# Performance work log

Hardware: AMD Instinct MI355X
Metric: run time of the kernel (lower is better)

## Reference

```python
import jax, jax.numpy as jnp
import numpy as np

N = 200000      # total nodes
E = 3200000     # total edges (avg degree 16)
B = 2000        # graphs
NPG = 100       # nodes per graph (N = B*NPG)
H = 32          # hidden_channels
MAXZ = 1000     # max_z
K = 60          # sort-pool k
D = H * 3 + 1   # total_latent_dim = 97
DENSE = ((K - 2) // 2 + 1 - 5 + 1) * 32  # 832


def setup_inputs() -> dict:
    key = jax.random.key(0)
    ks = jax.random.split(key, 24)
    inp = {}
    inp['z1'] = jax.random.randint(ks[0], (N,), 0, MAXZ)
    inp['z2'] = jax.random.randint(ks[1], (N,), 0, MAXZ)
    inp['w'] = jax.random.randint(ks[2], (N,), 0, MAXZ)
    inp['edge_index'] = jax.random.randint(ks[3], (2, E), 0, N)
    inp['batch'] = jnp.arange(N) // NPG  # contiguous graph ids
    inp['edge_weight'] = jax.random.uniform(ks[4], (E,), dtype=jnp.float32)
    s = 0.1
    inp['emb_w'] = jax.random.normal(ks[5], (MAXZ, H), jnp.float32) * s
    inp['emb_z1'] = jax.random.normal(ks[6], (MAXZ, H), jnp.float32) * s
    inp['emb_z2'] = jax.random.normal(ks[7], (MAXZ, H), jnp.float32) * s
    inp['W0'] = jax.random.normal(ks[8], (3 * H, H), jnp.float32) * s
    inp['b0'] = jnp.zeros((H,), jnp.float32)
    inp['W1'] = jax.random.normal(ks[9], (H, H), jnp.float32) * s
    inp['b1'] = jnp.zeros((H,), jnp.float32)
    inp['W2'] = jax.random.normal(ks[10], (H, H), jnp.float32) * s
    inp['b2'] = jnp.zeros((H,), jnp.float32)
    inp['W3'] = jax.random.normal(ks[11], (H, 1), jnp.float32) * s
    inp['b3'] = jnp.zeros((1,), jnp.float32)
    inp['c1_W'] = jax.random.normal(ks[12], (16, 1, D), jnp.float32) * s
    inp['c1_b'] = jnp.zeros((16,), jnp.float32)
    inp['c2_W'] = jax.random.normal(ks[13], (32, 16, 5), jnp.float32) * s
    inp['c2_b'] = jnp.zeros((32,), jnp.float32)
    inp['l1_W'] = jax.random.normal(ks[14], (DENSE, 128), jnp.float32) * s
    inp['l1_b'] = jnp.zeros((128,), jnp.float32)
    inp['l2_W'] = jax.random.normal(ks[15], (128, 1), jnp.float32) * s
    inp['l2_b'] = jnp.zeros((1,), jnp.float32)
    return inp


def _gcn(x, W, b, src, dst, ew):
    # GCNConv: add self loops (weight 1), symmetric normalization, aggregate src->dst
    loop = jnp.arange(N)
    s = jnp.concatenate([src, loop])
    d = jnp.concatenate([dst, loop])
    wgt = jnp.concatenate([ew, jnp.ones((N,), ew.dtype)])
    deg = jax.ops.segment_sum(wgt, d, num_segments=N)
    dis = jnp.where(deg > 0, jax.lax.rsqrt(deg), 0.0)
    norm = dis[s] * wgt * dis[d]
    h = x @ W                                  # [N, out]
    out = jax.ops.segment_sum(norm[:, None] * h[s], d, num_segments=N)
    return out + b


def reference(z1, z2, w, edge_index, batch, edge_weight,
              emb_w, emb_z1, emb_z2,
              W0, b0, W1, b1, W2, b2, W3, b3,
              c1_W, c1_b, c2_W, c2_b, l1_W, l1_b, l2_W, l2_b):
    src, dst = edge_index[0], edge_index[1]
    x0 = jnp.concatenate([emb_w[w], emb_z1[z1], emb_z2[z2]], axis=1)  # [N, 3H]
    h1 = jnp.tanh(_gcn(x0, W0, b0, src, dst, edge_weight))
    h2 = jnp.tanh(_gcn(h1, W1, b1, src, dst, edge_weight))
    h3 = jnp.tanh(_gcn(h2, W2, b2, src, dst, edge_weight))
    h4 = jnp.tanh(_gcn(h3, W3, b3, src, dst, edge_weight))
    x = jnp.concatenate([h1, h2, h3, h4], axis=-1)  # [N, D]

    # global_sort_pool: contiguous equal-size graphs -> reshape, sort desc by last channel, top-k
    xg = x.reshape(B, NPG, D)
    order = jnp.argsort(-xg[..., -1], axis=1)[:, :K]          # [B, K]
    xk = jnp.take_along_axis(xg, order[..., None], axis=1)    # [B, K, D]

    # conv1: kernel=stride=D on flattened [B,1,K*D] == per-slot projection
    t = jax.nn.relu(jnp.einsum('bkd,od->bok', xk, c1_W[:, 0, :]) + c1_b[None, :, None])  # [B,16,K]
    t = t.reshape(B, 16, K // 2, 2).max(axis=-1)              # maxpool 2,2 -> [B,16,30]
    t = jax.lax.conv_general_dilated(t, c2_W, (1,), 'VALID',
                                     dimension_numbers=('NCH', 'OIH', 'NCH'))
    t = jax.nn.relu(t + c2_b[None, :, None])                  # [B,32,26]
    t = t.reshape(B, -1)                                      # [B, DENSE]
    t = jax.nn.relu(t @ l1_W + l1_b)
    # dropout p=0.5 skipped (eval mode)
    return t @ l2_W + l2_b                                    # [B,1]
```

## Files before the change

kernel.cpp:

```cpp
#include <hip/hip_runtime.h>
#include <math.h>

#define NPG 100
#define KTOP 60
#define DLAT 97
#define NB 2000
#define NBLK 128
#define CPB 25000

static __device__ __forceinline__ float dot4(float4 a, float4 b){
  return a.x*b.x + a.y*b.y + a.z*b.z + a.w*b.w;
}

__global__ __launch_bounds__(256) void k_hist(const int* __restrict__ dst, int* __restrict__ histG, int E){
  __shared__ int h[NB];
  int blk = blockIdx.x, tid = threadIdx.x;
  for(int i=tid;i<NB;i+=256) h[i]=0;
  __syncthreads();
  int e0 = blk*CPB, e1 = min(e0+CPB, E);
  for(int e=e0+tid; e<e1; e+=256) atomicAdd(&h[dst[e]/NPG], 1);
  __syncthreads();
  for(int i=tid;i<NB;i+=256) histG[blk*NB+i] = h[i];
}

__global__ __launch_bounds__(NBLK) void k_colscan(const int* __restrict__ histG,
    int* __restrict__ prefT, int* __restrict__ total){
  __shared__ int s[NBLK];
  int b = blockIdx.x, t = threadIdx.x;
  int v = histG[t*NB + b];
  s[t] = v;
  __syncthreads();
  for(int off=1; off<NBLK; off<<=1){
    int u = (t >= off) ? s[t-off] : 0;
    __syncthreads();
    s[t] += u;
    __syncthreads();
  }
  prefT[b*NBLK + t] = s[t] - v;
  if(t == NBLK-1) total[b] = s[t];
}

__global__ __launch_bounds__(1024) void k_bscan(const int* __restrict__ total, int* __restrict__ bbase){
  __shared__ int s[1024];
  int t = threadIdx.x;
  int i0 = 2*t, i1 = 2*t+1;
  int x0 = (i0 < NB) ? total[i0] : 0;
  int x1 = (i1 < NB) ? total[i1] : 0;
  int ps = x0 + x1;
  s[t] = ps;
  __syncthreads();
  for(int off=1; off<1024; off<<=1){
    int u = (t >= off) ? s[t-off] : 0;
    __syncthreads();
    s[t] += u;
    __syncthreads();
  }
  int excl = s[t] - ps;
  if(i0 < NB) bbase[i0] = excl;
  if(i1 < NB) bbase[i1] = excl + x0;
  if(t == 1023) bbase[NB] = s[1023];
}

__global__ __launch_bounds__(256) void k_scatter(const int* __restrict__ src, const int* __restrict__ dst,
    const float* __restrict__ ew, const int* __restrict__ prefT, const int* __restrict__ bbase,
    int2* __restrict__ ebuf, int E){
  __shared__ int cur[NB];
  int blk = blockIdx.x, tid = threadIdx.x;
  for(int i=tid;i<NB;i+=256) cur[i] = prefT[i*NBLK + blk] + bbase[i];
  __syncthreads();
  int e0 = blk*CPB, e1 = min(e0+CPB, E);
  for(int e=e0+tid; e<e1; e+=256){
    int d = dst[e];
    int b = d/NPG;
    int dmod = d - b*NPG;
    int pos = atomicAdd(&cur[b], 1);
    ebuf[pos] = make_int2(src[e] | (dmod<<18), __float_as_int(ew[e]));
  }
}

__global__ __launch_bounds__(256) void k_bucket(const int2* __restrict__ ebuf, const int* __restrict__ bbase,
    float* __restrict__ dis, int* __restrict__ rs, int2* __restrict__ csr, int N){
  __shared__ float degw[NPG];
  __shared__ int cnt[NPG];
  __shared__ int cur[NPG];
  __shared__ int sc[128];
  int g = blockIdx.x, tid = threadIdx.x;
  int g0 = g*NPG;
  if(tid < NPG){ degw[tid] = 0.f; cnt[tid] = 0; }
  __syncthreads();
  int e0 = bbase[g], e1 = bbase[g+1];
  for(int e=e0+tid; e<e1; e+=256){
    int2 t = ebuf[e];
    int ld = ((unsigned)t.x)>>18;
    atomicAdd(&cnt[ld], 1);
    atomicAdd(&degw[ld], __int_as_float(t.y));
  }
  __syncthreads();
  if(tid < NPG) dis[g0+tid] = rsqrtf(degw[tid] + 1.0f);
  if(tid < 128) sc[tid] = (tid < NPG) ? cnt[tid] : 0;
  __syncthreads();
  for(int off=1; off<128; off<<=1){
    int u = 0;
    if(tid < 128 && tid >= off) u = sc[tid-off];
    __syncthreads();
    if(tid < 128) sc[tid] += u;
    __syncthreads();
  }
  if(tid < NPG){
    int st = e0 + sc[tid] - cnt[tid];
    cur[tid] = st;
    rs[g0+tid] = st;
  }
  if(g == NB-1 && tid == 0) rs[N] = e1;
  __syncthreads();
  for(int e=e0+tid; e<e1; e+=256){
    int2 t = ebuf[e];
    int ld = ((unsigned)t.x)>>18;
    int pos = atomicAdd(&cur[ld], 1);
    csr[pos] = make_int2(t.x & 0x3FFFF, t.y);
  }
}

__global__ __launch_bounds__(256) void k_gemm1(const int* __restrict__ wI, const int* __restrict__ z1I,
   const int* __restrict__ z2I,
   const float* __restrict__ embw, const float* __restrict__ embz1, const float* __restrict__ embz2,
   const float* __restrict__ W0, const float* __restrict__ dis, float* __restrict__ gx, int N){
  __shared__ __align__(16) float X[128][97];
  __shared__ __align__(16) float Ws[96*32];
  __shared__ int iw[128], i1[128], i2[128];
  int tid = threadIdx.x;
  int g0 = blockIdx.x*128;
  for(int i=tid;i<768;i+=256) ((float4*)Ws)[i] = ((const float4*)W0)[i];
  if(tid < 128){
    int gn = g0 + tid;
    bool ok = gn < N;
    iw[tid] = ok ? wI[gn]  : 0;
    i1[tid] = ok ? z1I[gn] : 0;
    i2[tid] = ok ? z2I[gn] : 0;
  }
  __syncthreads();
  for(int r=0;r<48;r++){
    int flat = r*256 + tid;
    int n = flat/96, c = flat - n*96;
    int gn = g0 + n;
    float val = 0.f;
    if(gn < N){
      if(c < 32)      val = embw [iw[n]*32 + c];
      else if(c < 64) val = embz1[i1[n]*32 + (c-32)];
      else            val = embz2[i2[n]*32 + (c-64)];
    }
    X[n][c] = val;
  }
  __syncthreads();
  int ng = tid>>3, chg = tid&7;
  float4 acc[4];
  #pragma unroll
  for(int j=0;j<4;j++) acc[j] = make_float4(0.f,0.f,0.f,0.f);
  #pragma unroll 4
  for(int i=0;i<96;i++){
    float4 wv = *(const float4*)&Ws[i*32 + chg*4];
    #pragma unroll
    for(int j=0;j<4;j++){
      float xv = X[ng*4+j][i];
      acc[j].x += xv*wv.x; acc[j].y += xv*wv.y; acc[j].z += xv*wv.z; acc[j].w += xv*wv.w;
    }
  }
  #pragma unroll
  for(int j=0;j<4;j++){
    int gn = g0 + ng*4 + j;
    if(gn < N){
      float dv = dis[gn];
      acc[j].x *= dv; acc[j].y *= dv; acc[j].z *= dv; acc[j].w *= dv;
      *(float4*)&gx[(size_t)gn*32 + chg*4] = acc[j];
    }
  }
}

__global__ __launch_bounds__(256) void k_gemm32(const float* __restrict__ xin, const float* __restrict__ W,
    const float* __restrict__ dis, float* __restrict__ gx, int N){
  __shared__ __align__(16) float X[128][33];
  __shared__ __align__(16) float Ws[32*32];
  int tid = threadIdx.x;
  int g0 = blockIdx.x*128;
  ((float4*)Ws)[tid] = ((const float4*)W)[tid];
  for(int r=0;r<4;r++){
    int f = r*256 + tid;
    int n = f>>3, c4 = f&7;
    int gn = g0 + n;
    float4 v = (gn < N) ? ((const float4*)(xin + (size_t)gn*32))[c4] : make_float4(0,0,0,0);
    float* xr = &X[n][c4*4];
    xr[0]=v.x; xr[1]=v.y; xr[2]=v.z; xr[3]=v.w;
  }
  __syncthreads();
  int ng = tid>>3, chg = tid&7;
  float4 acc[4];
  #pragma unroll
  for(int j=0;j<4;j++) acc[j] = make_float4(0.f,0.f,0.f,0.f);
  #pragma unroll 4
  for(int i=0;i<32;i++){
    float4 wv = *(const float4*)&Ws[i*32 + chg*4];
    #pragma unroll
    for(int j=0;j<4;j++){
      float xv = X[ng*4+j][i];
      acc[j].x += xv*wv.x; acc[j].y += xv*wv.y; acc[j].z += xv*wv.z; acc[j].w += xv*wv.w;
    }
  }
  #pragma unroll
  for(int j=0;j<4;j++){
    int gn = g0 + ng*4 + j;
    if(gn < N){
      float dv = dis[gn];
      acc[j].x *= dv; acc[j].y *= dv; acc[j].z *= dv; acc[j].w *= dv;
      *(float4*)&gx[(size_t)gn*32 + chg*4] = acc[j];
    }
  }
}

__global__ __launch_bounds__(256) void k_gemmv(const float* __restrict__ xin, const float* __restrict__ W3,
    const float* __restrict__ dis, float* __restrict__ gv, int N){
  __shared__ float X[256][33];
  __shared__ float Ws[32];
  int tid = threadIdx.x;
  int g0 = blockIdx.x*256;
  if(tid < 32) Ws[tid] = W3[tid];
  for(int r=0;r<8;r++){
    int f = r*256 + tid;
    int n = f>>3, c4 = f&7;
    int gn = g0 + n;
    float4 v = (gn < N) ? ((const float4*)(xin + (size_t)gn*32))[c4] : make_float4(0,0,0,0);
    float* xr = &X[n][c4*4];
    xr[0]=v.x; xr[1]=v.y; xr[2]=v.z; xr[3]=v.w;
  }
  __syncthreads();
  float acc = 0.f;
  #pragma unroll
  for(int i=0;i<32;i++) acc += X[tid][i]*Ws[i];
  int gn = g0 + tid;
  if(gn < N) gv[gn] = acc*dis[gn];
}

__global__ __launch_bounds__(256) void k_agg32(const float* __restrict__ g,
   const float* __restrict__ dis, const int* __restrict__ rs, const int2* __restrict__ csr,
   const float* __restrict__ bias, float* __restrict__ hout, int N){
  int wave = threadIdx.x >> 6;
  int lane = threadIdx.x & 63;
  int es = lane >> 3;
  int cg = lane & 7;
  int n = blockIdx.x*4 + wave;
  if(n >= N) return;
  int e0 = rs[n], e1 = rs[n+1];
  int deg = e1 - e0;
  int full = deg >> 3, rem = deg & 7;
  float4 acc = make_float4(0.f,0.f,0.f,0.f);
  int idx = e0 + es;
  for(int it=0; it<full; ++it){
    int2 p = csr[idx];
    float w = __int_as_float(p.y);
    float4 v = ((const float4*)(g + (size_t)p.x*32))[cg];
    acc.x += w*v.x; acc.y += w*v.y; acc.z += w*v.z; acc.w += w*v.w;
    idx += 8;
  }
  if(es < rem){
    int2 p = csr[idx];
    float w = __int_as_float(p.y);
    float4 v = ((const float4*)(g + (size_t)p.x*32))[cg];
    acc.x += w*v.x; acc.y += w*v.y; acc.z += w*v.z; acc.w += w*v.w;
  }
  #pragma unroll
  for(int off=8; off<64; off<<=1){
    acc.x += __shfl_xor(acc.x, off);
    acc.y += __shfl_xor(acc.y, off);
    acc.z += __shfl_xor(acc.z, off);
    acc.w += __shfl_xor(acc.w, off);
  }
  float4 self = ((const float4*)(g + (size_t)n*32))[cg];
  float dn = dis[n];
  float4 bv = ((const float4*)bias)[cg];
  if(es == 0){
    float4 o;
    o.x = tanhf(dn*(acc.x + self.x) + bv.x);
    o.y = tanhf(dn*(acc.y + self.y) + bv.y);
    o.z = tanhf(dn*(acc.z + self.z) + bv.z);
    o.w = tanhf(dn*(acc.w + self.w) + bv.w);
    ((float4*)(hout + (size_t)n*32))[cg] = o;
  }
}

__global__ void k_agg1(const float* __restrict__ gv, const float* __restrict__ dis,
   const int* __restrict__ rs, const int2* __restrict__ csr,
   const float* __restrict__ b3, float* __restrict__ h4, int N){
  int n = blockIdx.x*256 + threadIdx.x;
  if(n >= N) return;
  float acc = gv[n];
  int e0 = rs[n], e1 = rs[n+1];
  for(int e=e0;e<e1;e++){
    int2 p = csr[e];
    acc += __int_as_float(p.y)*gv[p.x];
  }
  h4[n] = tanhf(dis[n]*acc + b3[0]);
}

__global__ __launch_bounds__(256) void k_sortpool(const float* __restrict__ h1,const float* __restrict__ h2,
  const float* __restrict__ h3,const float* __restrict__ h4,
  const float* __restrict__ c1W,const float* __restrict__ c1b,
  float* __restrict__ t2G, int N){
  __shared__ float v[128];
  __shared__ int ord[KTOP];
  __shared__ __align__(16) float xk[KTOP][100];
  __shared__ __align__(16) float c1Ws[16*100];
  __shared__ __align__(16) float t2s[480];
  int b = blockIdx.x, tid = threadIdx.x;
  int g0 = b*NPG;
  for(int i=tid;i<16*97;i+=256){ int o=i/97, d=i-o*97; c1Ws[o*100+d]=c1W[i]; }
  if(tid < 100) v[tid] = h4[g0+tid];
  __syncthreads();
  if(tid < 100){
    float vi = v[tid];
    int rank = 0;
    for(int j=0;j<100;j++){
      float vj = v[j];
      rank += (vj > vi) || (vj == vi && j < tid);
    }
    if(rank < KTOP) ord[rank] = tid;
  }
  __syncthreads();
  for(int idx=tid; idx<KTOP*DLAT; idx+=256){
    int k = idx/DLAT, d = idx - k*DLAT;
    int n = g0 + ord[k];
    float val;
    if(d < 96){
      const float* hsrc = (d<32) ? h1 : (d<64) ? h2 : h3;
      val = hsrc[(size_t)n*32 + (d&31)];
    } else val = h4[n];
    xk[k][d] = val;
  }
  __syncthreads();
  {
    int og = tid & 7, j = tid >> 3;
    if(j < 30){
      int k0 = 2*j, k1 = 2*j+1;
      float a00=0.f, a01=0.f, a10=0.f, a11=0.f;
      for(int d=0; d<96; d+=4){
        float4 w0 = *(const float4*)&c1Ws[og*100 + d];
        float4 w1 = *(const float4*)&c1Ws[(og+8)*100 + d];
        float4 x0 = *(const float4*)&xk[k0][d];
        float4 x1 = *(const float4*)&xk[k1][d];
        a00 += dot4(x0, w0); a01 += dot4(x1, w0);
        a10 += dot4(x0, w1); a11 += dot4(x1, w1);
      }
      {
        float w0 = c1Ws[og*100 + 96], w1 = c1Ws[(og+8)*100 + 96];
        float x0 = xk[k0][96], x1 = xk[k1][96];
        a00 += x0*w0; a01 += x1*w0;
        a10 += x0*w1; a11 += x1*w1;
      }
      float b0v = c1b[og], b1v = c1b[og+8];
      float r0 = fmaxf(fmaxf(a00+b0v,0.f), fmaxf(a01+b0v,0.f));
      float r1 = fmaxf(fmaxf(a10+b1v,0.f), fmaxf(a11+b1v,0.f));
      t2s[og*30 + j] = r0;
      t2s[(og+8)*30 + j] = r1;
    }
  }
  __syncthreads();
  if(tid < 120) ((float4*)&t2G[(size_t)b*480])[tid] = ((const float4*)t2s)[tid];
}

__global__ __launch_bounds__(256) void k_tail(const float* __restrict__ t2G,
  const float* __restrict__ c2W,const float* __restrict__ c2b,
  const float* __restrict__ l1W,const float* __restrict__ l1b,
  const float* __restrict__ l2W,const float* __restrict__ l2b,
  float* __restrict__ out){
  __shared__ __align__(16) float t2s[8*480];
  __shared__ __align__(16) float c2Ws[2560];
  __shared__ __align__(16) float flat[8][832];
  __shared__ __align__(16) float o1s[8][128];
  int bG = blockIdx.x, tid = threadIdx.x;
  for(int i=tid; i<960; i+=256) ((float4*)t2s)[i] = ((const float4*)(t2G + (size_t)bG*8*480))[i];
  for(int i=tid; i<640; i+=256) ((float4*)c2Ws)[i] = ((const float4*)c2W)[i];
  __syncthreads();
  {
    int g = tid >> 5, oc = tid & 31;
    float acc[26];
    #pragma unroll
    for(int p=0;p<26;p++) acc[p]=0.f;
    for(int ic=0; ic<16; ic++){
      const float* trow = &t2s[g*480 + ic*30];
      float t[30];
      #pragma unroll
      for(int p=0;p<30;p++) t[p] = trow[p];
      const float* wr = &c2Ws[(oc*16 + ic)*5];
      float w0=wr[0], w1=wr[1], w2=wr[2], w3=wr[3], w4=wr[4];
      #pragma unroll
      for(int p=0;p<26;p++)
        acc[p] += t[p]*w0 + t[p+1]*w1 + t[p+2]*w2 + t[p+3]*w3 + t[p+4]*w4;
    }
    float bb = c2b[oc];
    #pragma unroll
    for(int p=0;p<26;p++) flat[g][oc*26+p] = fmaxf(acc[p]+bb, 0.f);
  }
  __syncthreads();
  {
    int j = tid & 127, gq = tid >> 7;
    float acc0=0.f, acc1=0.f, acc2=0.f, acc3=0.f;
    const float* f0 = flat[gq*4+0];
    const float* f1 = flat[gq*4+1];
    const float* f2 = flat[gq*4+2];
    const float* f3 = flat[gq*4+3];
    for(int i4=0; i4<208; i4++){
      int i = i4*4;
      float w0 = l1W[(size_t)i*128 + j];
      float w1 = l1W[(size_t)(i+1)*128 + j];
      float w2 = l1W[(size_t)(i+2)*128 + j];
      float w3 = l1W[(size_t)(i+3)*128 + j];
      float4 a0 = *(const float4*)&f0[i];
      float4 a1 = *(const float4*)&f1[i];
      float4 a2 = *(const float4*)&f2[i];
      float4 a3 = *(const float4*)&f3[i];
      acc0 += a0.x*w0 + a0.y*w1 + a0.z*w2 + a0.w*w3;
      acc1 += a1.x*w0 + a1.y*w1 + a1.z*w2 + a1.w*w3;
      acc2 += a2.x*w0 + a2.y*w1 + a2.z*w2 + a2.w*w3;
      acc3 += a3.x*w0 + a3.y*w1 + a3.z*w2 + a3.w*w3;
    }
    o1s[gq*4+0][j] = acc0;
    o1s[gq*4+1][j] = acc1;
    o1s[gq*4+2][j] = acc2;
    o1s[gq*4+3][j] = acc3;
  }
  __syncthreads();
  {
    int g = tid >> 5, jj = tid & 31;
    float s = 0.f;
    #pragma unroll
    for(int q=0;q<4;q++){
      int j = jj + 32*q;
      float r = fmaxf(o1s[g][j] + l1b[j], 0.f);
      s += r * l2W[j];
    }
    #pragma unroll
    for(int off=16; off>0; off>>=1) s += __shfl_xor(s, off);
    if(jj == 0) out[bG*8 + g] = s + l2b[0];
  }
}

extern "C" void kernel_launch(void* const* d_in, const int* in_sizes, int n_in,
                              void* d_out, int out_size, void* d_ws, size_t ws_size,
                              hipStream_t stream){
  (void)n_in; (void)out_size; (void)ws_size;
  const int*   z1    = (const int*)  d_in[0];
  const int*   z2    = (const int*)  d_in[1];
  const int*   w     = (const int*)  d_in[2];
  const int*   eidx  = (const int*)  d_in[3];
  const float* ew    = (const float*)d_in[5];
  const float* embw  = (const float*)d_in[6];
  const float* embz1 = (const float*)d_in[7];
  const float* embz2 = (const float*)d_in[8];
  const float* W0    = (const float*)d_in[9];
  const float* b0    = (const float*)d_in[10];
  const float* W1    = (const float*)d_in[11];
  const float* b1    = (const float*)d_in[12];
  const float* W2    = (const float*)d_in[13];
  const float* b2    = (const float*)d_in[14];
  const float* W3    = (const float*)d_in[15];
  const float* b3    = (const float*)d_in[16];
  const float* c1W   = (const float*)d_in[17];
  const float* c1b   = (const float*)d_in[18];
  const float* c2W   = (const float*)d_in[19];
  const float* c2b   = (const float*)d_in[20];
  const float* l1W   = (const float*)d_in[21];
  const float* l1b   = (const float*)d_in[22];
  const float* l2W   = (const float*)d_in[23];
  const float* l2b   = (const float*)d_in[24];
  float* out = (float*)d_out;

  int N = in_sizes[0];
  int E = in_sizes[3]/2;
  int B = N/NPG;
  const int* src = eidx;
  const int* dst = eidx + E;

  char* p = (char*)d_ws;
  auto alloc = [&](size_t bytes)->char*{
    char* r = p;
    p += (bytes + 255) & ~(size_t)255;
    return r;
  };
  float* h1    = (float*)alloc((size_t)N*32*4);
  float* h2    = (float*)alloc((size_t)N*32*4);
  float* h3    = (float*)alloc((size_t)N*32*4);
  float* h4    = (float*)alloc((size_t)N*4);
  float* gx    = (float*)alloc((size_t)N*32*4);
  float* dis   = (float*)alloc((size_t)N*4);
  int*   rs    = (int*)  alloc((size_t)(N+1)*4);
  int*   histG = (int*)  alloc((size_t)NBLK*NB*4);
  int*   prefT = (int*)  alloc((size_t)NB*NBLK*4);
  int*   total = (int*)  alloc((size_t)NB*4);
  int*   bbase = (int*)  alloc((size_t)(NB+1)*4);
  int2*  csr   = (int2*) alloc((size_t)E*8);
  float* t2G   = (float*)alloc((size_t)B*480*4);
  int2*  ebuf  = (int2*)h1;

  k_hist   <<<NBLK, 256, 0, stream>>>(dst, histG, E);
  k_colscan<<<NB,  NBLK, 0, stream>>>(histG, prefT, total);
  k_bscan  <<<1,   1024, 0, stream>>>(total, bbase);
  k_scatter<<<NBLK, 256, 0, stream>>>(src, dst, ew, prefT, bbase, ebuf, E);
  k_bucket <<<B,    256, 0, stream>>>(ebuf, bbase, dis, rs, csr, N);

  int gG = (N+127)/128;
  int gA = (N+3)/4;
  k_gemm1 <<<gG, 256, 0, stream>>>(w, z1, z2, embw, embz1, embz2, W0, dis, gx, N);
  k_agg32 <<<gA, 256, 0, stream>>>(gx, dis, rs, csr, b0, h1, N);
  k_gemm32<<<gG, 256, 0, stream>>>(h1, W1, dis, gx, N);
  k_agg32 <<<gA, 256, 0, stream>>>(gx, dis, rs, csr, b1, h2, N);
  k_gemm32<<<gG, 256, 0, stream>>>(h2, W2, dis, gx, N);
  k_agg32 <<<gA, 256, 0, stream>>>(gx, dis, rs, csr, b2, h3, N);
  k_gemmv <<<(N+255)/256, 256, 0, stream>>>(h3, W3, dis, gx, N);
  k_agg1  <<<(N+255)/256, 256, 0, stream>>>(gx, dis, rs, csr, b3, h4, N);

  k_sortpool<<<B, 256, 0, stream>>>(h1, h2, h3, h4, c1W, c1b, t2G, N);
  k_tail    <<<B/8, 256, 0, stream>>>(t2G, c2W, c2b, l1W, l1b, l2W, l2b, out);
}
```

Baseline: 809.8 us.

## Coarsen CSR build buckets to 800-node chunks with more scatter blocks

The two-level counting sort that builds the CSR now buckets edges into 250 chunks of 800 nodes instead of 2000 per-graph buckets. This lets the histogram and scatter passes run across 1024 blocks instead of 128, with much smaller shared histograms, so more of the GPU is used. The second-level bucket kernel then handles 800 nodes per 1024-thread block, with a longer in-block scan. In exchange there is more shared-atomic contention per bucket in the scatter pass and fewer blocks in the final bucketing pass.

```diff
diff --git a/kernel.cpp b/kernel.cpp
--- a/kernel.cpp
+++ b/kernel.cpp
@@ -4,117 +4,112 @@
 #define NPG 100
 #define KTOP 60
 #define DLAT 97
-#define NB 2000
-#define NBLK 128
-#define CPB 25000
+#define NC 250
+#define NODESC 800
+#define NBLKA 1024
 
 static __device__ __forceinline__ float dot4(float4 a, float4 b){
   return a.x*b.x + a.y*b.y + a.z*b.z + a.w*b.w;
 }
 
-__global__ __launch_bounds__(256) void k_hist(const int* __restrict__ dst, int* __restrict__ histG, int E){
-  __shared__ int h[NB];
+__global__ __launch_bounds__(256) void k_histA(const int* __restrict__ dst, int* __restrict__ histA,
+    int E, int cpb){
+  __shared__ int h[NC];
   int blk = blockIdx.x, tid = threadIdx.x;
-  for(int i=tid;i<NB;i+=256) h[i]=0;
-  __syncthreads();
-  int e0 = blk*CPB, e1 = min(e0+CPB, E);
-  for(int e=e0+tid; e<e1; e+=256) atomicAdd(&h[dst[e]/NPG], 1);
-  __syncthreads();
-  for(int i=tid;i<NB;i+=256) histG[blk*NB+i] = h[i];
-}
-
-__global__ __launch_bounds__(NBLK) void k_colscan(const int* __restrict__ histG,
-    int* __restrict__ prefT, int* __restrict__ total){
-  __shared__ int s[NBLK];
-  int b = blockIdx.x, t = threadIdx.x;
-  int v = histG[t*NB + b];
+  if(tid < NC) h[tid] = 0;
+  __syncthreads();
+  int e0 = blk*cpb, e1 = min(e0+cpb, E);
+  for(int e=e0+tid; e<e1; e+=256) atomicAdd(&h[dst[e]/NODESC], 1);
+  __syncthreads();
+  if(tid < NC) histA[blk*NC + tid] = h[tid];
+}
+
+__global__ __launch_bounds__(NBLKA) void k_colscanA(const int* __restrict__ histA,
+    int* __restrict__ prefA, int* __restrict__ totalA){
+  __shared__ int s[NBLKA];
+  int c = blockIdx.x, t = threadIdx.x;
+  int v = histA[t*NC + c];
   s[t] = v;
   __syncthreads();
-  for(int off=1; off<NBLK; off<<=1){
+  for(int off=1; off<NBLKA; off<<=1){
     int u = (t >= off) ? s[t-off] : 0;
     __syncthreads();
     s[t] += u;
     __syncthreads();
   }
-  prefT[b*NBLK + t] = s[t] - v;
-  if(t == NBLK-1) total[b] = s[t];
-}
-
-__global__ __launch_bounds__(1024) void k_bscan(const int* __restrict__ total, int* __restrict__ bbase){
-  __shared__ int s[1024];
+  prefA[c*NBLKA + t] = s[t] - v;
+  if(t == NBLKA-1) totalA[c] = s[t];
+}
+
+__global__ __launch_bounds__(256) void k_bscanA(const int* __restrict__ totalA, int* __restrict__ cbase){
+  __shared__ int s[256];
   int t = threadIdx.x;
-  int i0 = 2*t, i1 = 2*t+1;
-  int x0 = (i0 < NB) ? total[i0] : 0;
-  int x1 = (i1 < NB) ? total[i1] : 0;
-  int ps = x0 + x1;
-  s[t] = ps;
-  __syncthreads();
-  for(int off=1; off<1024; off<<=1){
+  int v = (t < NC) ? totalA[t] : 0;
+  s[t] = v;
+  __syncthreads();
+  for(int off=1; off<256; off<<=1){
     int u = (t >= off) ? s[t-off] : 0;
     __syncthreads();
     s[t] += u;
     __syncthreads();
   }
-  int excl = s[t] - ps;
-  if(i0 < NB) bbase[i0] = excl;
-  if(i1 < NB) bbase[i1] = excl + x0;
-  if(t == 1023) bbase[NB] = s[1023];
-}
-
-__global__ __launch_bounds__(256) void k_scatter(const int* __restrict__ src, const int* __restrict__ dst,
-    const float* __restrict__ ew, const int* __restrict__ prefT, const int* __restrict__ bbase,
-    int2* __restrict__ ebuf, int E){
-  __shared__ int cur[NB];
+  if(t < NC) cbase[t] = s[t] - v;
+  if(t == 255) cbase[NC] = s[255];
+}
+
+__global__ __launch_bounds__(256) void k_scatterA(const int* __restrict__ src, const int* __restrict__ dst,
+    const float* __restrict__ ew, const int* __restrict__ prefA, const int* __restrict__ cbase,
+    int2* __restrict__ ebufA, int E, int cpb){
+  __shared__ int cur[NC];
   int blk = blockIdx.x, tid = threadIdx.x;
-  for(int i=tid;i<NB;i+=256) cur[i] = prefT[i*NBLK + blk] + bbase[i];
-  __syncthreads();
-  int e0 = blk*CPB, e1 = min(e0+CPB, E);
+  if(tid < NC) cur[tid] = prefA[tid*NBLKA + blk] + cbase[tid];
+  __syncthreads();
+  int e0 = blk*cpb, e1 = min(e0+cpb, E);
   for(int e=e0+tid; e<e1; e+=256){
     int d = dst[e];
-    int b = d/NPG;
-    int dmod = d - b*NPG;
-    int pos = atomicAdd(&cur[b], 1);
-    ebuf[pos] = make_int2(src[e] | (dmod<<18), __float_as_int(ew[e]));
-  }
-}
-
-__global__ __launch_bounds__(256) void k_bucket(const int2* __restrict__ ebuf, const int* __restrict__ bbase,
+    int c = d/NODESC;
+    int dm = d - c*NODESC;
+    int pos = atomicAdd(&cur[c], 1);
+    ebufA[pos] = make_int2(src[e] | (dm<<18), __float_as_int(ew[e]));
+  }
+}
+
+__global__ __launch_bounds__(1024) void k_bucket8(const int2* __restrict__ ebufA, const int* __restrict__ cbase,
     float* __restrict__ dis, int* __restrict__ rs, int2* __restrict__ csr, int N){
-  __shared__ float degw[NPG];
-  __shared__ int cnt[NPG];
-  __shared__ int cur[NPG];
-  __shared__ int sc[128];
-  int g = blockIdx.x, tid = threadIdx.x;
-  int g0 = g*NPG;
-  if(tid < NPG){ degw[tid] = 0.f; cnt[tid] = 0; }
-  __syncthreads();
-  int e0 = bbase[g], e1 = bbase[g+1];
-  for(int e=e0+tid; e<e1; e+=256){
-    int2 t = ebuf[e];
+  __shared__ float degw[NODESC];
+  __shared__ int cnt[NODESC];
+  __shared__ int cur[NODESC];
+  __shared__ int sc[1024];
+  int c = blockIdx.x, tid = threadIdx.x;
+  int n0 = c*NODESC;
+  if(tid < NODESC){ degw[tid] = 0.f; cnt[tid] = 0; }
+  __syncthreads();
+  int e0 = cbase[c], e1 = cbase[c+1];
+  for(int e=e0+tid; e<e1; e+=1024){
+    int2 t = ebufA[e];
     int ld = ((unsigned)t.x)>>18;
     atomicAdd(&cnt[ld], 1);
     atomicAdd(&degw[ld], __int_as_float(t.y));
   }
   __syncthreads();
-  if(tid < NPG) dis[g0+tid] = rsqrtf(degw[tid] + 1.0f);
-  if(tid < 128) sc[tid] = (tid < NPG) ? cnt[tid] : 0;
-  __syncthreads();
-  for(int off=1; off<128; off<<=1){
-    int u = 0;
-    if(tid < 128 && tid >= off) u = sc[tid-off];
+  if(tid < NODESC) dis[n0+tid] = rsqrtf(degw[tid] + 1.0f);
+  sc[tid] = (tid < NODESC) ? cnt[tid] : 0;
+  __syncthreads();
+  for(int off=1; off<1024; off<<=1){
+    int u = (tid >= off) ? sc[tid-off] : 0;
     __syncthreads();
-    if(tid < 128) sc[tid] += u;
+    sc[tid] += u;
     __syncthreads();
   }
-  if(tid < NPG){
+  if(tid < NODESC){
     int st = e0 + sc[tid] - cnt[tid];
     cur[tid] = st;
-    rs[g0+tid] = st;
-  }
-  if(g == NB-1 && tid == 0) rs[N] = e1;
-  __syncthreads();
-  for(int e=e0+tid; e<e1; e+=256){
-    int2 t = ebuf[e];
+    rs[n0+tid] = st;
+  }
+  if(c == NC-1 && tid == 0) rs[N] = e1;
+  __syncthreads();
+  for(int e=e0+tid; e<e1; e+=1024){
+    int2 t = ebufA[e];
     int ld = ((unsigned)t.x)>>18;
     int pos = atomicAdd(&cur[ld], 1);
     csr[pos] = make_int2(t.x & 0x3FFFF, t.y);
@@ -491,19 +486,20 @@
   float* gx    = (float*)alloc((size_t)N*32*4);
   float* dis   = (float*)alloc((size_t)N*4);
   int*   rs    = (int*)  alloc((size_t)(N+1)*4);
-  int*   histG = (int*)  alloc((size_t)NBLK*NB*4);
-  int*   prefT = (int*)  alloc((size_t)NB*NBLK*4);
-  int*   total = (int*)  alloc((size_t)NB*4);
-  int*   bbase = (int*)  alloc((size_t)(NB+1)*4);
+  int*   histA = (int*)  alloc((size_t)NBLKA*NC*4);
+  int*   prefA = (int*)  alloc((size_t)NC*NBLKA*4);
+  int*   totalA= (int*)  alloc((size_t)NC*4);
+  int*   cbase = (int*)  alloc((size_t)(NC+1)*4);
   int2*  csr   = (int2*) alloc((size_t)E*8);
   float* t2G   = (float*)alloc((size_t)B*480*4);
-  int2*  ebuf  = (int2*)h1;
-
-  k_hist   <<<NBLK, 256, 0, stream>>>(dst, histG, E);
-  k_colscan<<<NB,  NBLK, 0, stream>>>(histG, prefT, total);
-  k_bscan  <<<1,   1024, 0, stream>>>(total, bbase);
-  k_scatter<<<NBLK, 256, 0, stream>>>(src, dst, ew, prefT, bbase, ebuf, E);
-  k_bucket <<<B,    256, 0, stream>>>(ebuf, bbase, dis, rs, csr, N);
+  int2*  ebufA = (int2*)h1;
+
+  int cpb = (E + NBLKA - 1)/NBLKA;
+  k_histA   <<<NBLKA, 256, 0, stream>>>(dst, histA, E, cpb);
+  k_colscanA<<<NC, NBLKA, 0, stream>>>(histA, prefA, totalA);
+  k_bscanA  <<<1,    256, 0, stream>>>(totalA, cbase);
+  k_scatterA<<<NBLKA, 256, 0, stream>>>(src, dst, ew, prefA, cbase, ebufA, E, cpb);
+  k_bucket8 <<<NC,  1024, 0, stream>>>(ebufA, cbase, dis, rs, csr, N);
 
   int gG = (N+127)/128;
   int gA = (N+3)/4;
```

After: 722.8 us. 1.12x faster.
